# Optimization experiments

Hardware: AMD Instinct MI355X
Metric: run time of the kernel (lower is better)

Reference implementation:

```python
import jax, jax.numpy as jnp
import numpy as np

NUM_LAYERS = 3
NORM = True


def wl_refine(colors, src, dst, n):
    """One WLConv step: new color = first-occurrence rank of the signature
    (own_color, sorted multiset of in-neighbor colors). Exact partition match
    with PyG WLConv (fresh hashmap per layer, as each conv is called once)."""
    nbr = colors[src]                                  # [E] neighbor colors grouped by dst
    deg = jnp.zeros((n,), jnp.int32).at[dst].add(1)    # in-degree
    maxdeg = int(deg.max())
    order = jnp.lexsort((nbr, dst))                    # sort edges by (dst, nbr_color)
    d_s, c_s = dst[order], nbr[order]
    offsets = jnp.cumsum(deg) - deg                    # start of each node's edge block
    pos = jnp.arange(d_s.shape[0]) - offsets[d_s]      # rank within block (already color-sorted)
    mat = jnp.full((n, maxdeg), -1, colors.dtype).at[d_s, pos].set(c_s)
    keys = jnp.concatenate([colors[:, None], mat], axis=1)  # [n, maxdeg+1] signatures
    uniq, first, inv = jnp.unique(keys, axis=0, return_index=True, return_inverse=True)
    inv = inv.reshape(-1)
    rank = jnp.argsort(jnp.argsort(first))             # unique-id -> first-occurrence order id
    return rank[inv], int(uniq.shape[0])


def histogram(colors, num_colors, batch, bsize, weights, norm):
    """PyG WLConv.histogram: scatter counts into [bsize, num_colors], L2-normalize rows."""
    idx = batch * num_colors + colors
    out = jnp.zeros((bsize * num_colors,), weights.dtype).at[idx].add(weights)
    out = out.reshape(bsize, num_colors)
    if norm:
        out = out / jnp.linalg.norm(out, axis=-1, keepdims=True)
    return out


def setup_inputs() -> dict:
    key = jax.random.key(0)
    k1, k2, k3 = jax.random.split(key, 3)
    N, E, B, C0 = 100000, 3200000, 512, 32
    x = jax.random.randint(k1, (N,), 0, C0)
    edge_index = jax.random.randint(k2, (2, E), 0, N)
    batch = jnp.sort(jax.random.randint(k3, (N,), 0, B))
    node_weight = jnp.ones((N,), jnp.float32)
    return {"x": x, "edge_index": edge_index, "batch": batch, "node_weight": node_weight}


def reference(x, edge_index, batch, node_weight):
    src, dst = edge_index[0], edge_index[1]            # PyG WLConv: neighbors of i = sources of edges into i
    n = x.shape[0]
    bsize = int(batch.max()) + 1
    colors = x
    hists = []
    for _ in range(NUM_LAYERS):
        colors, nc = wl_refine(colors, src, dst, n)
        hists.append(histogram(colors, nc, batch, bsize, node_weight, NORM))
    return tuple(hists)
```

## Files before the change

kernel.cpp:

```cpp
#include <hip/hip_runtime.h>
#include <math.h>

#define WL_LAYERS 3
#define HSLOTS (1u << 18)
#define HMASK  (HSLOTS - 1u)
#define SCHUNK 1024
#define MAXD 128

typedef unsigned long long u64;
typedef int v4i __attribute__((ext_vector_type(4)));

__device__ __forceinline__ u64 mix64(u64 x) {
    x += 0x9e3779b97f4a7c15ULL;
    x = (x ^ (x >> 30)) * 0xbf58476d1ce4e5b9ULL;
    x = (x ^ (x >> 27)) * 0x94d049bb133111ebULL;
    return x ^ (x >> 31);
}

__device__ __forceinline__ void nt_fill(float* __restrict__ zbuf, long long a4,
                                        long long b4, long long tid, long long T) {
    v4i z = {0, 0, 0, 0};
    v4i* z4 = (v4i*)zbuf;
    for (long long j = a4 + tid; j < b4; j += T)
        __builtin_nontemporal_store(z, &z4[j]);
}

__global__ void k_setup(int* __restrict__ cursor, u64* __restrict__ ktab0,
                        int* __restrict__ gmin0, float* __restrict__ sumsq0,
                        int* __restrict__ dcnt, long long* __restrict__ scalars,
                        float* __restrict__ zbuf, long long a4e, long long zn, int n) {
    long long tid = (long long)blockIdx.x * blockDim.x + threadIdx.x;
    long long T = (long long)gridDim.x * blockDim.x;
    for (long long j = tid; j < n; j += T) cursor[j] = 0;
    for (long long j = tid; j < (long long)HSLOTS; j += T) { ktab0[j] = 0ULL; gmin0[j] = 0x7fffffff; }
    for (long long j = tid; j < n; j += T) sumsq0[j] = 0.f;
    if (tid < 8) dcnt[tid] = 0;
    if (tid == 0) scalars[3] = 0;
    nt_fill(zbuf, 0, a4e, tid, T);
    long long n4 = zn >> 2;
    if (tid < (zn & 3)) zbuf[(n4 << 2) + tid] = 0.f;
}

__global__ void k_scatter(const int* __restrict__ src, const int* __restrict__ dst,
                          int* __restrict__ cursor, int* __restrict__ adj,
                          float* __restrict__ zbuf, long long a4, long long b4, int E) {
    long long tid = (long long)blockIdx.x * blockDim.x + threadIdx.x;
    long long T = (long long)gridDim.x * blockDim.x;
    if ((E & 3) == 0) {
        int nE4 = E >> 2;
        if (tid < nE4) {
            v4i s4 = ((const v4i*)src)[tid];
            v4i d4 = ((const v4i*)dst)[tid];
#pragma unroll
            for (int j = 0; j < 4; ++j) {
                int d = d4[j];
                int pos = atomicAdd(&cursor[d], 1);
                if (pos < MAXD) adj[(size_t)d * MAXD + pos] = s4[j];
            }
        }
    } else {
        for (long long e = tid; e < E; e += T) {
            int d = dst[e];
            int pos = atomicAdd(&cursor[d], 1);
            if (pos < MAXD) adj[(size_t)d * MAXD + pos] = src[e];
        }
    }
    nt_fill(zbuf, a4, b4, tid, T);
}

__device__ __forceinline__ void hash_insert_body(
        const int* __restrict__ col, const int* __restrict__ cursor,
        const int* __restrict__ adj, u64* __restrict__ ktab, int* __restrict__ gmin,
        int* __restrict__ nodeslot, int n) {
    int i = blockIdx.x * 256 + threadIdx.x;
    if (i >= n) return;
    int dg = cursor[i]; if (dg > MAXD) dg = MAXD;
    const int* row = adj + (size_t)i * MAXD;
    u64 h = 0ULL;
    int dg4 = dg >> 2;
    const v4i* row4 = (const v4i*)row;
    for (int k4 = 0; k4 < dg4; ++k4) {
        v4i r = row4[k4];
#pragma unroll
        for (int j = 0; j < 4; ++j) {
            u64 c = (u64)(unsigned)col[r[j]];
            h += mix64(c ^ 0x5bf03635c1d4aeb1ULL);
        }
    }
    for (int k = dg4 << 2; k < dg; ++k) {
        u64 c = (u64)(unsigned)col[row[k]];
        h += mix64(c ^ 0x5bf03635c1d4aeb1ULL);
    }
    u64 bb = mix64((u64)(unsigned)col[i] + 0x0123456789abcdefULL);
    u64 cc = mix64((u64)(unsigned)dg + 0xfedcba9876543210ULL);
    u64 sig = mix64(h + bb * 0x9e3779b97f4a7c15ULL + cc * 0xc2b2ae3d27d4eb4fULL);
    if (!sig) sig = 1;
    unsigned slot = (unsigned)sig & HMASK;
    for (;;) {
        u64 p = atomicCAS(&ktab[slot], 0ULL, sig);
        if (p == 0ULL || p == sig) break;
        slot = (slot + 1) & HMASK;
    }
    nodeslot[i] = slot;
    atomicMin(&gmin[slot], i);
}

__global__ void k_hashinsert(const int* __restrict__ col, const int* __restrict__ cursor,
                             const int* __restrict__ adj, u64* __restrict__ ktab,
                             int* __restrict__ gmin, int* __restrict__ nodeslot,
                             float* __restrict__ zbuf, long long b4, long long n4, int n) {
    long long tid = (long long)blockIdx.x * 256 + threadIdx.x;
    nt_fill(zbuf, b4, n4, tid, (long long)gridDim.x * 256);
    hash_insert_body(col, cursor, adj, ktab, gmin, nodeslot, n);
}

__global__ void k_scanF(const int* __restrict__ nodeslot, const int* __restrict__ gmin,
                        int* __restrict__ rankv, int* __restrict__ bsum,
                        int* __restrict__ dcnt, long long* __restrict__ scalars,
                        int layer, const int* __restrict__ batch, int n, int nb) {
    __shared__ int s[256];
    __shared__ int sh_last;
    int t = threadIdx.x;
    int idx0 = blockIdx.x * SCHUNK + t * 4;
    int v[4]; int sum = 0;
#pragma unroll
    for (int j = 0; j < 4; ++j) {
        int ii = idx0 + j;
        v[j] = (ii < n && gmin[nodeslot[ii]] == ii) ? 1 : 0;
        sum += v[j];
    }
    s[t] = sum; __syncthreads();
    for (int off = 1; off < 256; off <<= 1) {
        int x = (t >= off) ? s[t - off] : 0;
        __syncthreads(); s[t] += x; __syncthreads();
    }
    int run = s[t] - sum;
#pragma unroll
    for (int j = 0; j < 4; ++j) { int ii = idx0 + j; if (ii < n) rankv[ii] = run; run += v[j]; }
    if (t == 255) bsum[blockIdx.x] = s[255];
    __threadfence();
    if (t == 0) sh_last = (atomicAdd(&dcnt[0], 1) == gridDim.x - 1);
    __syncthreads();
    if (sh_last) {
        __threadfence();
        int v2 = (t < nb) ? bsum[t] : 0;
        __syncthreads();
        s[t] = v2; __syncthreads();
        for (int off = 1; off < 256; off <<= 1) {
            int x = (t >= off) ? s[t - off] : 0;
            __syncthreads(); s[t] += x; __syncthreads();
        }
        if (t < nb) bsum[t] = s[t] - v2;
        if (t == 255) {
            long long total = s[255];
            scalars[layer] = total;
            long long bsize = (long long)batch[n - 1] + 1;
            scalars[4 + layer] = scalars[3 + layer] + bsize * total;
        }
    }
}

__global__ void k_hist(const int* __restrict__ batch, const int* __restrict__ nodeslot,
                       const int* __restrict__ gmin, const int* __restrict__ rankv,
                       const int* __restrict__ bsum, int* __restrict__ nxt,
                       const float* __restrict__ w, float* __restrict__ out,
                       float* __restrict__ sumsq, float* __restrict__ oldv,
                       const long long* __restrict__ scalars, int layer,
                       u64* __restrict__ ktabN, int* __restrict__ gminN,
                       float* __restrict__ sumsqN, int zeroNext, int n) {
    __shared__ float ssq[64];
    __shared__ int rbase_s;
    int t = threadIdx.x;
    int i = blockIdx.x * 256 + t;
    if (zeroNext) {
        int tid = i, T = gridDim.x * 256;
        for (int j = tid; j < (int)HSLOTS; j += T) { ktabN[j] = 0ULL; gminN[j] = 0x7fffffff; }
        for (int j = tid; j < n; j += T) sumsqN[j] = 0.f;
    }
    if (t < 64) ssq[t] = 0.f;
    if (t == 0) {
        int a = blockIdx.x * 256;
        rbase_s = batch[a < n ? a : n - 1];
    }
    __syncthreads();
    if (i < n) {
        int g = gmin[nodeslot[i]];
        int c = rankv[g] + bsum[g >> 10];
        nxt[i] = c;
        int r = batch[i];
        long long idx = scalars[3 + layer] + (long long)r * scalars[layer] + c;
        float wi = w[i];
        float old = atomicAdd(&out[idx], wi);
        oldv[i] = old;
        float val = 2.f * old * wi + wi * wi;
        int sl = r - rbase_s;
        if (sl >= 0 && sl < 64) atomicAdd(&ssq[sl], val);
        else atomicAdd(&sumsq[r], val);
    }
    __syncthreads();
    if (t < 64 && ssq[t] != 0.f) atomicAdd(&sumsq[rbase_s + t], ssq[t]);
}

__global__ void k_normhash(
        const int* __restrict__ batch, const int* __restrict__ col,
        float* __restrict__ out, const float* __restrict__ sumsq_prev,
        const float* __restrict__ oldv, const long long* __restrict__ scalars,
        int layerPrev, const int* __restrict__ cursor, const int* __restrict__ adj,
        u64* __restrict__ ktab, int* __restrict__ gmin, int* __restrict__ nodeslot,
        int n) {
    int i = blockIdx.x * 256 + threadIdx.x;
    if (i < n && oldv[i] == 0.f) {
        int r = batch[i];
        long long idx = scalars[3 + layerPrev] + (long long)r * scalars[layerPrev] + col[i];
        out[idx] = out[idx] / sqrtf(sumsq_prev[r]);
    }
    hash_insert_body(col, cursor, adj, ktab, gmin, nodeslot, n);
}

__global__ void k_norm(const int* __restrict__ batch, const int* __restrict__ col,
                       float* __restrict__ out, const float* __restrict__ sumsq,
                       const float* __restrict__ oldv,
                       const long long* __restrict__ scalars, int layer, int n) {
    int i = blockIdx.x * blockDim.x + threadIdx.x;
    if (i >= n) return;
    if (oldv[i] != 0.f) return;
    int r = batch[i];
    long long idx = scalars[3 + layer] + (long long)r * scalars[layer] + col[i];
    out[idx] = out[idx] / sqrtf(sumsq[r]);
}

extern "C" void kernel_launch(void* const* d_in, const int* in_sizes, int n_in,
                              void* d_out, int out_size, void* d_ws, size_t ws_size,
                              hipStream_t stream) {
    const int* x = (const int*)d_in[0];
    const int* ei = (const int*)d_in[1];
    const int* batch = (const int*)d_in[2];
    const float* w = (const float*)d_in[3];
    int N = in_sizes[0];
    int E = in_sizes[1] / 2;
    const int* src = ei;
    const int* dst = ei + E;

    char* p = (char*)d_ws;
    u64* ktabs = (u64*)p;               p += (size_t)3 * HSLOTS * 8;
    long long* scalars = (long long*)p; p += 8 * 8;
    int* adj      = (int*)p;            p += (size_t)N * MAXD * 4;
    int* gmins    = (int*)p;            p += (size_t)3 * HSLOTS * 4;
    int* cursor   = (int*)p;            p += (size_t)N * 4;
    int* nodeslot = (int*)p;            p += (size_t)N * 4;
    int* rankv    = (int*)p;            p += (size_t)N * 4;
    int* colA     = (int*)p;            p += (size_t)N * 4;
    int* colB     = (int*)p;            p += (size_t)N * 4;
    float* oldv   = (float*)p;          p += (size_t)N * 4;
    float* sumsqs = (float*)p;          p += (size_t)3 * N * 4;
    int* bsum     = (int*)p;            p += 256 * 4;
    int* dcnt     = (int*)p;            p += 8 * 4;
    if ((size_t)(p - (char*)d_ws) > ws_size) return;

    int gN = (N + 255) / 256;
    int gE = (E + 255) / 256;
    int gE4 = ((E + 3) / 4 + 255) / 256;
    int nb = (N + SCHUNK - 1) / SCHUNK;
    if (nb > 256) return;

    float* out = (float*)d_out;
    long long zn = (long long)out_size;
    long long n4 = zn >> 2;
    long long A = (n4 * 3) / 10;
    long long B = (n4 * 9) / 10;

    k_setup<<<gE, 256, 0, stream>>>(cursor, ktabs, gmins, sumsqs, dcnt, scalars,
                                    out, A, zn, N);
    k_scatter<<<gE4, 256, 0, stream>>>(src, dst, cursor, adj, out, A, B, E);
    k_hashinsert<<<gN, 256, 0, stream>>>(x, cursor, adj, ktabs, gmins, nodeslot,
                                         out, B, n4, N);

    int* nxt = colA;
    for (int l = 0; l < WL_LAYERS; ++l) {
        u64* kt = ktabs + (size_t)l * HSLOTS;
        int* gm = gmins + (size_t)l * HSLOTS;
        float* sq = sumsqs + (size_t)l * N;
        int zeroNext = (l < WL_LAYERS - 1) ? 1 : 0;
        k_scanF<<<nb, 256, 0, stream>>>(nodeslot, gm, rankv, bsum, dcnt + l,
                                        scalars, l, batch, N, nb);
        k_hist<<<gN, 256, 0, stream>>>(batch, nodeslot, gm, rankv, bsum, nxt, w,
                                       out, sq, oldv, scalars, l,
                                       kt + HSLOTS, gm + HSLOTS, sq + N, zeroNext, N);
        if (l < WL_LAYERS - 1) {
            k_normhash<<<gN, 256, 0, stream>>>(batch, nxt, out, sq, oldv,
                                               scalars, l, cursor, adj,
                                               kt + HSLOTS, gm + HSLOTS, nodeslot, N);
        } else {
            k_norm<<<gN, 256, 0, stream>>>(batch, nxt, out, sq, oldv, scalars, l, N);
        }
        nxt = (l == 0) ? colB : colA;
    }
}
```

Baseline: 383.7 us.

## Fuse histogram and row normalization into one per-graph block kernel

```diff
diff --git a/kernel.cpp b/kernel.cpp
--- a/kernel.cpp
+++ b/kernel.cpp
@@ -25,15 +25,20 @@
         __builtin_nontemporal_store(z, &z4[j]);
 }
 
+__device__ __forceinline__ int lbound(const int* __restrict__ a, int n, int key) {
+    int lo = 0, hi = n;
+    while (lo < hi) { int mid = (lo + hi) >> 1; if (a[mid] < key) lo = mid + 1; else hi = mid; }
+    return lo;
+}
+
 __global__ void k_setup(int* __restrict__ cursor, u64* __restrict__ ktab0,
-                        int* __restrict__ gmin0, float* __restrict__ sumsq0,
-                        int* __restrict__ dcnt, long long* __restrict__ scalars,
+                        int* __restrict__ gmin0, int* __restrict__ dcnt,
+                        long long* __restrict__ scalars,
                         float* __restrict__ zbuf, long long a4e, long long zn, int n) {
     long long tid = (long long)blockIdx.x * blockDim.x + threadIdx.x;
     long long T = (long long)gridDim.x * blockDim.x;
     for (long long j = tid; j < n; j += T) cursor[j] = 0;
     for (long long j = tid; j < (long long)HSLOTS; j += T) { ktab0[j] = 0ULL; gmin0[j] = 0x7fffffff; }
-    for (long long j = tid; j < n; j += T) sumsq0[j] = 0.f;
     if (tid < 8) dcnt[tid] = 0;
     if (tid == 0) scalars[3] = 0;
     nt_fill(zbuf, 0, a4e, tid, T);
@@ -108,9 +113,11 @@
 __global__ void k_hashinsert(const int* __restrict__ col, const int* __restrict__ cursor,
                              const int* __restrict__ adj, u64* __restrict__ ktab,
                              int* __restrict__ gmin, int* __restrict__ nodeslot,
-                             float* __restrict__ zbuf, long long b4, long long n4, int n) {
-    long long tid = (long long)blockIdx.x * 256 + threadIdx.x;
-    nt_fill(zbuf, b4, n4, tid, (long long)gridDim.x * 256);
+                             float* __restrict__ zbuf, long long b4, long long e4, int n) {
+    if (e4 > b4) {
+        long long tid = (long long)blockIdx.x * 256 + threadIdx.x;
+        nt_fill(zbuf, b4, e4, tid, (long long)gridDim.x * 256);
+    }
     hash_insert_body(col, cursor, adj, ktab, gmin, nodeslot, n);
 }
 
@@ -160,73 +167,49 @@
     }
 }
 
-__global__ void k_hist(const int* __restrict__ batch, const int* __restrict__ nodeslot,
-                       const int* __restrict__ gmin, const int* __restrict__ rankv,
-                       const int* __restrict__ bsum, int* __restrict__ nxt,
-                       const float* __restrict__ w, float* __restrict__ out,
-                       float* __restrict__ sumsq, float* __restrict__ oldv,
-                       const long long* __restrict__ scalars, int layer,
-                       u64* __restrict__ ktabN, int* __restrict__ gminN,
-                       float* __restrict__ sumsqN, int zeroNext, int n) {
-    __shared__ float ssq[64];
-    __shared__ int rbase_s;
+__global__ void __launch_bounds__(512) k_histnorm(
+        const int* __restrict__ batch, const int* __restrict__ nodeslot,
+        const int* __restrict__ gmin, const int* __restrict__ rankv,
+        const int* __restrict__ bsum, int* __restrict__ nxt,
+        const float* __restrict__ w, float* __restrict__ out,
+        float* __restrict__ oldv, const long long* __restrict__ scalars, int layer,
+        u64* __restrict__ ktabN, int* __restrict__ gminN, int zeroNext, int n) {
+    __shared__ int rs_s, re_s, bsize_s;
+    __shared__ float ssq;
     int t = threadIdx.x;
-    int i = blockIdx.x * 256 + t;
     if (zeroNext) {
-        int tid = i, T = gridDim.x * 256;
+        int tid = blockIdx.x * 512 + t, T = gridDim.x * 512;
         for (int j = tid; j < (int)HSLOTS; j += T) { ktabN[j] = 0ULL; gminN[j] = 0x7fffffff; }
-        for (int j = tid; j < n; j += T) sumsqN[j] = 0.f;
-    }
-    if (t < 64) ssq[t] = 0.f;
-    if (t == 0) {
-        int a = blockIdx.x * 256;
-        rbase_s = batch[a < n ? a : n - 1];
-    }
+    }
+    long long nc = scalars[layer];
+    long long base = scalars[3 + layer];
+    if (t == 0) bsize_s = batch[n - 1] + 1;
     __syncthreads();
-    if (i < n) {
-        int g = gmin[nodeslot[i]];
-        int c = rankv[g] + bsum[g >> 10];
-        nxt[i] = c;
-        int r = batch[i];
-        long long idx = scalars[3 + layer] + (long long)r * scalars[layer] + c;
-        float wi = w[i];
-        float old = atomicAdd(&out[idx], wi);
-        oldv[i] = old;
-        float val = 2.f * old * wi + wi * wi;
-        int sl = r - rbase_s;
-        if (sl >= 0 && sl < 64) atomicAdd(&ssq[sl], val);
-        else atomicAdd(&sumsq[r], val);
-    }
-    __syncthreads();
-    if (t < 64 && ssq[t] != 0.f) atomicAdd(&sumsq[rbase_s + t], ssq[t]);
-}
-
-__global__ void k_normhash(
-        const int* __restrict__ batch, const int* __restrict__ col,
-        float* __restrict__ out, const float* __restrict__ sumsq_prev,
-        const float* __restrict__ oldv, const long long* __restrict__ scalars,
-        int layerPrev, const int* __restrict__ cursor, const int* __restrict__ adj,
-        u64* __restrict__ ktab, int* __restrict__ gmin, int* __restrict__ nodeslot,
-        int n) {
-    int i = blockIdx.x * 256 + threadIdx.x;
-    if (i < n && oldv[i] == 0.f) {
-        int r = batch[i];
-        long long idx = scalars[3 + layerPrev] + (long long)r * scalars[layerPrev] + col[i];
-        out[idx] = out[idx] / sqrtf(sumsq_prev[r]);
-    }
-    hash_insert_body(col, cursor, adj, ktab, gmin, nodeslot, n);
-}
-
-__global__ void k_norm(const int* __restrict__ batch, const int* __restrict__ col,
-                       float* __restrict__ out, const float* __restrict__ sumsq,
-                       const float* __restrict__ oldv,
-                       const long long* __restrict__ scalars, int layer, int n) {
-    int i = blockIdx.x * blockDim.x + threadIdx.x;
-    if (i >= n) return;
-    if (oldv[i] != 0.f) return;
-    int r = batch[i];
-    long long idx = scalars[3 + layer] + (long long)r * scalars[layer] + col[i];
-    out[idx] = out[idx] / sqrtf(sumsq[r]);
+    int bsize = bsize_s;
+    for (int r = blockIdx.x; r < bsize; r += gridDim.x) {
+        __syncthreads();
+        if (t == 0) { rs_s = lbound(batch, n, r); re_s = lbound(batch, n, r + 1); ssq = 0.f; }
+        __syncthreads();
+        int rs = rs_s, re = re_s;
+        long long rowb = base + (long long)r * nc;
+        for (int i = rs + t; i < re; i += 512) {
+            int g = gmin[nodeslot[i]];
+            int c = rankv[g] + bsum[g >> 10];
+            nxt[i] = c;
+            float wi = w[i];
+            float old = atomicAdd(&out[rowb + c], wi);
+            oldv[i] = old;
+            atomicAdd(&ssq, 2.f * old * wi + wi * wi);
+        }
+        __syncthreads();
+        float denom = sqrtf(ssq);
+        for (int i = rs + t; i < re; i += 512) {
+            if (oldv[i] != 0.f) continue;
+            long long idx = rowb + nxt[i];
+            float cv = atomicAdd(&out[idx], 0.f);
+            out[idx] = cv / denom;
+        }
+    }
 }
 
 extern "C" void kernel_launch(void* const* d_in, const int* in_sizes, int n_in,
@@ -252,7 +235,6 @@
     int* colA     = (int*)p;            p += (size_t)N * 4;
     int* colB     = (int*)p;            p += (size_t)N * 4;
     float* oldv   = (float*)p;          p += (size_t)N * 4;
-    float* sumsqs = (float*)p;          p += (size_t)3 * N * 4;
     int* bsum     = (int*)p;            p += 256 * 4;
     int* dcnt     = (int*)p;            p += 8 * 4;
     if ((size_t)(p - (char*)d_ws) > ws_size) return;
@@ -269,8 +251,7 @@
     long long A = (n4 * 3) / 10;
     long long B = (n4 * 9) / 10;
 
-    k_setup<<<gE, 256, 0, stream>>>(cursor, ktabs, gmins, sumsqs, dcnt, scalars,
-                                    out, A, zn, N);
+    k_setup<<<gE, 256, 0, stream>>>(cursor, ktabs, gmins, dcnt, scalars, out, A, zn, N);
     k_scatter<<<gE4, 256, 0, stream>>>(src, dst, cursor, adj, out, A, B, E);
     k_hashinsert<<<gN, 256, 0, stream>>>(x, cursor, adj, ktabs, gmins, nodeslot,
                                          out, B, n4, N);
@@ -279,19 +260,16 @@
     for (int l = 0; l < WL_LAYERS; ++l) {
         u64* kt = ktabs + (size_t)l * HSLOTS;
         int* gm = gmins + (size_t)l * HSLOTS;
-        float* sq = sumsqs + (size_t)l * N;
         int zeroNext = (l < WL_LAYERS - 1) ? 1 : 0;
         k_scanF<<<nb, 256, 0, stream>>>(nodeslot, gm, rankv, bsum, dcnt + l,
                                         scalars, l, batch, N, nb);
-        k_hist<<<gN, 256, 0, stream>>>(batch, nodeslot, gm, rankv, bsum, nxt, w,
-                                       out, sq, oldv, scalars, l,
-                                       kt + HSLOTS, gm + HSLOTS, sq + N, zeroNext, N);
+        k_histnorm<<<512, 512, 0, stream>>>(batch, nodeslot, gm, rankv, bsum, nxt, w,
+                                            out, oldv, scalars, l,
+                                            kt + HSLOTS, gm + HSLOTS, zeroNext, N);
         if (l < WL_LAYERS - 1) {
-            k_normhash<<<gN, 256, 0, stream>>>(batch, nxt, out, sq, oldv,
-                                               scalars, l, cursor, adj,
-                                               kt + HSLOTS, gm + HSLOTS, nodeslot, N);
-        } else {
-            k_norm<<<gN, 256, 0, stream>>>(batch, nxt, out, sq, oldv, scalars, l, N);
+            k_hashinsert<<<gN, 256, 0, stream>>>(nxt, cursor, adj,
+                                                 kt + HSLOTS, gm + HSLOTS, nodeslot,
+                                                 out, 0, 0, N);
         }
         nxt = (l == 0) ? colB : colA;
     }
```

Result: slower. 404.5 us (+5.4%).
